# Kernel optimization log

Measured on AMD Instinct MI355X. Metric: run time of the kernel, lower is better.

Reference implementation:

```python
import jax, jax.numpy as jnp
import numpy as np

N = 20000      # nodes
E = 120000     # directed edges (self-loops added in reference, per PyG default)
F_IN = 235
HID = 256
HEADS = 8
NEG_SLOPE = 0.2


def setup_inputs() -> dict:
    key = jax.random.key(0)
    ks = jax.random.split(key, 24)
    p = lambda k, shape: (jax.random.normal(k, shape, jnp.float32) * 0.05)
    inp = {}
    inp["x"] = jax.random.normal(ks[0], (N, F_IN), jnp.float32)
    inp["edge_index"] = jax.random.randint(ks[1], (2, E), 0, N, jnp.int32)
    # input projection
    inp["w_in"] = p(ks[2], (F_IN, HID)); inp["b_in"] = jnp.zeros((HID,), jnp.float32)
    # temporal MLP
    inp["w_t1"] = p(ks[3], (HID, HID)); inp["b_t1"] = jnp.zeros((HID,), jnp.float32)
    inp["w_t2"] = p(ks[4], (HID, HID)); inp["b_t2"] = jnp.zeros((HID,), jnp.float32)
    # GAT layer 1: heads=8, out_per_head=32, concat -> 256
    C1 = HID // HEADS
    inp["w_g1"] = p(ks[5], (HID, HEADS * C1)); inp["a_src1"] = p(ks[6], (HEADS, C1))
    inp["a_dst1"] = p(ks[7], (HEADS, C1)); inp["b_g1"] = jnp.zeros((HEADS * C1,), jnp.float32)
    # GAT layer 2: same shape
    inp["w_g2"] = p(ks[8], (HID, HEADS * C1)); inp["a_src2"] = p(ks[9], (HEADS, C1))
    inp["a_dst2"] = p(ks[10], (HEADS, C1)); inp["b_g2"] = jnp.zeros((HEADS * C1,), jnp.float32)
    # GAT layer 3: heads=8, out_per_head=256, concat -> 2048
    inp["w_g3"] = p(ks[11], (HID, HEADS * HID)); inp["a_src3"] = p(ks[12], (HEADS, HID))
    inp["a_dst3"] = p(ks[13], (HEADS, HID)); inp["b_g3"] = jnp.zeros((HEADS * HID,), jnp.float32)
    # classifier
    inp["w_c1"] = p(ks[14], (2 * HID, HID)); inp["b_c1"] = jnp.zeros((HID,), jnp.float32)
    inp["w_c2"] = p(ks[15], (HID, 2)); inp["b_c2"] = jnp.zeros((2,), jnp.float32)
    return inp


def _gat(x, src, dst, W, a_src, a_dst, b, C):
    """PyG-style GATConv: gather -> per-edge logits -> segment softmax -> scatter-add."""
    h = (x @ W).reshape(-1, HEADS, C)                       # [N, H, C]
    alpha_s = jnp.sum(h * a_src, axis=-1)                   # [N, H]
    alpha_d = jnp.sum(h * a_dst, axis=-1)                   # [N, H]
    e = jax.nn.leaky_relu(alpha_s[src] + alpha_d[dst], NEG_SLOPE)   # [Etot, H]
    m = jax.ops.segment_max(e, dst, num_segments=N)         # [N, H] (self-loops ensure non-empty)
    ex = jnp.exp(e - m[dst])
    den = jax.ops.segment_sum(ex, dst, num_segments=N)
    alpha = ex / (den[dst] + 1e-16)                          # [Etot, H]
    out = jax.ops.segment_sum(alpha[:, :, None] * h[src], dst, num_segments=N)  # [N, H, C]
    return out.reshape(-1, HEADS * C) + b


def reference(x, edge_index, w_in, b_in, w_t1, b_t1, w_t2, b_t2,
              w_g1, a_src1, a_dst1, b_g1, w_g2, a_src2, a_dst2, b_g2,
              w_g3, a_src3, a_dst3, b_g3, w_c1, b_c1, w_c2, b_c2):
    h = jax.nn.elu(x @ w_in + b_in)                          # [N, 256]
    t = jax.nn.relu(h @ w_t1 + b_t1) @ w_t2 + b_t2          # [N, 256] (dropout inactive in eval)
    loop = jnp.arange(N, dtype=edge_index.dtype)
    src = jnp.concatenate([edge_index[0], loop])
    dst = jnp.concatenate([edge_index[1], loop])
    g = jax.nn.elu(_gat(h, src, dst, w_g1, a_src1, a_dst1, b_g1, HID // HEADS))
    g = jax.nn.elu(_gat(g, src, dst, w_g2, a_src2, a_dst2, b_g2, HID // HEADS))
    g = jax.nn.elu(_gat(g, src, dst, w_g3, a_src3, a_dst3, b_g3, HID))  # [N, 2048]
    g = g.reshape(N, HEADS, HID).mean(axis=1)                # [N, 256]
    comb = jnp.concatenate([g, t], axis=-1)                  # [N, 512]
    logits = jax.nn.relu(comb @ w_c1 + b_c1) @ w_c2 + b_c2   # [N, 2]
    return logits
```

## Files before the change

### kernel.cpp

```cpp
#include <hip/hip_runtime.h>
#include <hip/hip_bf16.h>
#include <math.h>


#define HID 256
#define HEADS 8
#define FIN 235

typedef __attribute__((ext_vector_type(8))) short short8;
typedef __attribute__((ext_vector_type(4))) float floatx4;

__device__ __forceinline__ float elu_f(float x) { return x > 0.f ? x : __expf(x) - 1.f; }
__device__ __forceinline__ float bf2f(unsigned short u) {
  return __uint_as_float(((unsigned int)u) << 16);
}
__device__ __forceinline__ unsigned short f2bfu(float f) {
  union { __hip_bfloat16 b; unsigned short u; } c;
  c.b = __float2bfloat16(f);
  return c.u;
}

__global__ void xcvt_k(const float* __restrict__ x, __hip_bfloat16* __restrict__ xb, int M) {
  int id = blockIdx.x * blockDim.x + threadIdx.x;
  if (id >= M * 256) return;
  int m = id >> 8, k = id & 255;
  xb[id] = (k < FIN) ? __float2bfloat16(x[(size_t)m * FIN + k]) : __float2bfloat16(0.f);
}

__global__ void wprep_k(const float* __restrict__ w_in, const float* __restrict__ w_t1,
                        const float* __restrict__ w_g1, const float* __restrict__ w_t2,
                        const float* __restrict__ w_g2, const float* __restrict__ w_c1,
                        const float* __restrict__ w_g3, const float* __restrict__ a_s3,
                        const float* __restrict__ a_d3, __hip_bfloat16* __restrict__ wtin,
                        __hip_bfloat16* __restrict__ wtpair, __hip_bfloat16* __restrict__ wtt2,
                        __hip_bfloat16* __restrict__ wtg2, __hip_bfloat16* __restrict__ wtc1,
                        __hip_bfloat16* __restrict__ wtg3s, float* __restrict__ apj) {
  __shared__ float t[32][33];
  int z = blockIdx.z;
  if (z == 14) {
    int idx = (blockIdx.y * 8 + blockIdx.x) * 256 + threadIdx.y * 32 + threadIdx.x;
    if (idx < 256 * 16) {
      int k = idx >> 4, o = idx & 15;
      int h = o >> 1;
      const float* av = (o & 1) ? (a_d3 + h * 256) : (a_s3 + h * 256);
      const float* wr = w_g3 + (size_t)k * 2048 + h * 256;
      float s = 0.f;
      for (int c = 0; c < 256; c++) s += wr[c] * av[c];
      apj[idx] = s;
    }
    return;
  }
  const float* src;
  __hip_bfloat16* dst;
  int K, Kpad, Nstride;
  if (z == 5) {
    src = w_c1; dst = wtc1; K = 512; Kpad = 512; Nstride = 256;
  } else {
    if (blockIdx.y >= 8) return;
    switch (z) {
      case 0: src = w_in; dst = wtin; K = FIN; Kpad = 256; Nstride = 256; break;
      case 1: src = w_t1; dst = wtpair; K = 256; Kpad = 256; Nstride = 256; break;
      case 2: src = w_g1; dst = wtpair + 256 * 256; K = 256; Kpad = 256; Nstride = 256; break;
      case 3: src = w_t2; dst = wtt2; K = 256; Kpad = 256; Nstride = 256; break;
      case 4: src = w_g2; dst = wtg2; K = 256; Kpad = 256; Nstride = 256; break;
      default: {
        int h = z - 6;
        src = w_g3 + h * 256; dst = wtg3s + h * 256; K = 256; Kpad = 2048; Nstride = 2048;
      }
    }
  }
  int nb = blockIdx.x * 32, kb = blockIdx.y * 32;
  int tx = threadIdx.x, ty = threadIdx.y;
#pragma unroll
  for (int j = 0; j < 32; j += 8) {
    int k = kb + ty + j;
    t[ty + j][tx] = (k < K) ? src[(size_t)k * Nstride + nb + tx] : 0.f;
  }
  __syncthreads();
#pragma unroll
  for (int j = 0; j < 32; j += 8) {
    int n = nb + ty + j;
    int k = kb + tx;
    dst[(size_t)n * Kpad + k] = __float2bfloat16(t[tx][ty + j]);
  }
}

__global__ void count_k(const int* __restrict__ ei, int* __restrict__ deg, int E) {
  int i = blockIdx.x * blockDim.x + threadIdx.x;
  if (i < E) atomicAdd(&deg[ei[E + i]], 1);
}

__global__ void scan_k(const int* __restrict__ deg, int* __restrict__ rp, int n) {
  __shared__ int wsum[16];
  __shared__ int s_carry;
  int tid = threadIdx.x, lane = tid & 63, wid = tid >> 6;
  if (tid == 0) { s_carry = 0; rp[0] = 0; }
  __syncthreads();
  for (int base = 0; base < n; base += 1024) {
    int i = base + tid;
    int x = (i < n) ? (deg[i] + 1) : 0;
#pragma unroll
    for (int off = 1; off < 64; off <<= 1) {
      int y = __shfl_up(x, off);
      if (lane >= off) x += y;
    }
    if (lane == 63) wsum[wid] = x;
    __syncthreads();
    if (wid == 0 && lane < 16) {
      int s = wsum[lane];
#pragma unroll
      for (int off = 1; off < 16; off <<= 1) {
        int y = __shfl_up(s, off);
        if (lane >= off) s += y;
      }
      wsum[lane] = s;
    }
    __syncthreads();
    int offset = s_carry + (wid > 0 ? wsum[wid - 1] : 0);
    if (i < n) rp[i + 1] = offset + x;
    __syncthreads();
    if (tid == 1023) s_carry += wsum[15];
    __syncthreads();
  }
}

__global__ void fill_k(const int* __restrict__ ei, const int* __restrict__ rp,
                       int* __restrict__ fillc, int* __restrict__ colA, int E, int n) {
  int i = blockIdx.x * blockDim.x + threadIdx.x;
  if (i < E) {
    int d = ei[E + i];
    int pos = rp[d] + atomicAdd(&fillc[d], 1);
    colA[pos] = ei[i];
  } else if (i < E + n) {
    int v = i - E;
    int pos = rp[v] + atomicAdd(&fillc[v], 1);
    colA[pos] = v;
  }
}

template <int ACT>
__global__ __launch_bounds__(256) void mgemm64_k(
    const __hip_bfloat16* __restrict__ A, const __hip_bfloat16* __restrict__ Bt,
    const float* __restrict__ bias, __hip_bfloat16* __restrict__ Cb,
    int ldc, int M, int N, int K) {
  __shared__ short As[64 * 40];
  __shared__ short Bs[64 * 40];
  int tid = threadIdx.x;
  int row0 = blockIdx.y * 64, col0 = blockIdx.x * 64;
  int w = tid >> 6, lane = tid & 63;
  int wr = w >> 1, wc = w & 1;
  int quad = lane >> 4, l16 = lane & 15;
  floatx4 zero = {0.f, 0.f, 0.f, 0.f};
  floatx4 acc[2][2];
#pragma unroll
  for (int i = 0; i < 2; i++)
#pragma unroll
    for (int j = 0; j < 2; j++) acc[i][j] = zero;

  int srow = tid >> 2, sq = tid & 3;
  const __hip_bfloat16* Ap = A + (size_t)(row0 + srow) * K + sq * 8;
  const __hip_bfloat16* Bp = Bt + (size_t)(col0 + srow) * K + sq * 8;
  bool aok = (row0 + srow) < M;

  uint4 a1 = make_uint4(0, 0, 0, 0);
  if (aok) a1 = *(const uint4*)(Ap);
  uint4 b1 = *(const uint4*)(Bp);

  for (int k0 = 0; k0 < K; k0 += 32) {
    __syncthreads();
    *(uint4*)&As[srow * 40 + sq * 8] = a1;
    *(uint4*)&Bs[srow * 40 + sq * 8] = b1;
    int kn = k0 + 32;
    if (kn < K) {
      if (aok) a1 = *(const uint4*)(Ap + kn);
      b1 = *(const uint4*)(Bp + kn);
    }
    __syncthreads();
    short8 fa[2], fb[2];
#pragma unroll
    for (int i = 0; i < 2; i++) {
      fa[i] = *(const short8*)&As[(wr * 32 + i * 16 + l16) * 40 + quad * 8];
      fb[i] = *(const short8*)&Bs[(wc * 32 + i * 16 + l16) * 40 + quad * 8];
    }
#pragma unroll
    for (int mi = 0; mi < 2; mi++)
#pragma unroll
      for (int ni = 0; ni < 2; ni++)
        acc[mi][ni] = __builtin_amdgcn_mfma_f32_16x16x32_bf16(fa[mi], fb[ni], acc[mi][ni], 0, 0, 0);
  }

#pragma unroll
  for (int mi = 0; mi < 2; mi++) {
    int rbase = row0 + wr * 32 + mi * 16 + quad * 4;
#pragma unroll
    for (int ni = 0; ni < 2; ni++) {
      int c = col0 + wc * 32 + ni * 16 + l16;
      float bv = bias ? bias[c] : 0.f;
#pragma unroll
      for (int reg = 0; reg < 4; reg++) {
        int rr = rbase + reg;
        if (rr >= M) continue;
        float v = acc[mi][ni][reg] + bv;
        if (ACT == 1) v = fmaxf(v, 0.f);
        if (ACT == 2) v = elu_f(v);
        Cb[(size_t)rr * ldc + c] = __float2bfloat16(v);
      }
    }
  }
}

__global__ __launch_bounds__(256) void mgemm_dual_k(
    const __hip_bfloat16* __restrict__ A, const __hip_bfloat16* __restrict__ Bt,
    const float* __restrict__ bias1, __hip_bfloat16* __restrict__ O1,
    __hip_bfloat16* __restrict__ O2, int M) {
  const int K = 256;
  __shared__ short As[64 * 40];
  __shared__ short Bs[128 * 40];
  int tid = threadIdx.x;
  int row0 = blockIdx.y * 64, col0 = blockIdx.x * 128;
  int w = tid >> 6, lane = tid & 63;
  int wr = w >> 1, wc = w & 1;
  int quad = lane >> 4, l16 = lane & 15;
  floatx4 zero = {0.f, 0.f, 0.f, 0.f};
  floatx4 acc[2][4];
#pragma unroll
  for (int i = 0; i < 2; i++)
#pragma unroll
    for (int j = 0; j < 4; j++) acc[i][j] = zero;

  int srow = tid >> 2, sq = tid & 3;
  const __hip_bfloat16* Ap = A + (size_t)(row0 + srow) * K + sq * 8;
  const __hip_bfloat16* Bp1 = Bt + (size_t)(col0 + srow) * K + sq * 8;
  const __hip_bfloat16* Bp2 = Bt + (size_t)(col0 + 64 + srow) * K + sq * 8;
  bool aok = (row0 + srow) < M;

  uint4 a1 = make_uint4(0, 0, 0, 0);
  if (aok) a1 = *(const uint4*)(Ap);
  uint4 b1 = *(const uint4*)(Bp1);
  uint4 b2 = *(const uint4*)(Bp2);

  for (int k0 = 0; k0 < K; k0 += 32) {
    __syncthreads();
    *(uint4*)&As[srow * 40 + sq * 8] = a1;
    *(uint4*)&Bs[srow * 40 + sq * 8] = b1;
    *(uint4*)&Bs[(64 + srow) * 40 + sq * 8] = b2;
    int kn = k0 + 32;
    if (kn < K) {
      if (aok) a1 = *(const uint4*)(Ap + kn);
      b1 = *(const uint4*)(Bp1 + kn);
      b2 = *(const uint4*)(Bp2 + kn);
    }
    __syncthreads();
    short8 fa[2], fb[4];
#pragma unroll
    for (int i = 0; i < 2; i++)
      fa[i] = *(const short8*)&As[(wr * 32 + i * 16 + l16) * 40 + quad * 8];
#pragma unroll
    for (int i = 0; i < 4; i++)
      fb[i] = *(const short8*)&Bs[(wc * 64 + i * 16 + l16) * 40 + quad * 8];
#pragma unroll
    for (int mi = 0; mi < 2; mi++)
#pragma unroll
      for (int ni = 0; ni < 4; ni++)
        acc[mi][ni] = __builtin_amdgcn_mfma_f32_16x16x32_bf16(fa[mi], fb[ni], acc[mi][ni], 0, 0, 0);
  }

#pragma unroll
  for (int mi = 0; mi < 2; mi++) {
    int rbase = row0 + wr * 32 + mi * 16 + quad * 4;
#pragma unroll
    for (int ni = 0; ni < 4; ni++) {
      int c = col0 + wc * 64 + ni * 16 + l16;
      bool first = c < 256;
      float bv = first ? bias1[c] : 0.f;
      int cc = first ? c : (c - 256);
#pragma unroll
      for (int reg = 0; reg < 4; reg++) {
        int rr = rbase + reg;
        if (rr >= M) continue;
        float v = acc[mi][ni][reg] + bv;
        if (first) v = fmaxf(v, 0.f);
        __hip_bfloat16* dst = first ? O1 : O2;
        dst[(size_t)rr * 256 + cc] = __float2bfloat16(v);
      }
    }
  }
}

__global__ __launch_bounds__(512) void mgemm3_k(
    const __hip_bfloat16* __restrict__ A, const __hip_bfloat16* __restrict__ Bt,
    const float* __restrict__ bias, __hip_bfloat16* __restrict__ comb, int M) {
  const int K = 2048;
  __shared__ short As[64 * 40];
  __shared__ short Bs[256 * 40];
  int tid = threadIdx.x;
  int row0 = blockIdx.x * 64;
  int w = tid >> 6, lane = tid & 63;
  int wr = w & 3, wc = w >> 2;
  int quad = lane >> 4, l16 = lane & 15;
  floatx4 acc[8], sum[8];
#pragma unroll
  for (int i = 0; i < 8; i++) {
    acc[i] = (floatx4){0.f, 0.f, 0.f, 0.f};
    sum[i] = (floatx4){0.f, 0.f, 0.f, 0.f};
  }

  bool at = tid < 256;
  int arow = tid >> 2, achk = (tid & 3) * 8;
  const __hip_bfloat16* Ap = A + (size_t)(row0 + arow) * K + achk;
  bool aok = at && (row0 + arow) < M;
  int brow = tid >> 1, boff = (tid & 1) * 16;
  const __hip_bfloat16* Bp = Bt + (size_t)brow * K + boff;

  uint4 a1 = make_uint4(0, 0, 0, 0);
  if (aok) a1 = *(const uint4*)(Ap);
  uint4 b1 = *(const uint4*)(Bp);
  uint4 b2 = *(const uint4*)(Bp + 8);

  for (int k0 = 0; k0 < K; k0 += 32) {
    __syncthreads();
    if (at) *(uint4*)&As[arow * 40 + achk] = a1;
    *(uint4*)&Bs[brow * 40 + boff] = b1;
    *(uint4*)&Bs[brow * 40 + boff + 8] = b2;
    int kn = k0 + 32;
    if (kn < K) {
      if (aok) a1 = *(const uint4*)(Ap + kn);
      b1 = *(const uint4*)(Bp + kn);
      b2 = *(const uint4*)(Bp + kn + 8);
    }
    __syncthreads();
    short8 fa = *(const short8*)&As[(wr * 16 + l16) * 40 + quad * 8];
#pragma unroll
    for (int ni = 0; ni < 8; ni++) {
      short8 fb = *(const short8*)&Bs[(wc * 128 + ni * 16 + l16) * 40 + quad * 8];
      acc[ni] = __builtin_amdgcn_mfma_f32_16x16x32_bf16(fa, fb, acc[ni], 0, 0, 0);
    }
    if (((k0 + 32) & 255) == 0) {
      int h = k0 >> 8;
#pragma unroll
      for (int ni = 0; ni < 8; ni++) {
        int c = wc * 128 + ni * 16 + l16;
        float bv = bias[h * 256 + c];
#pragma unroll
        for (int reg = 0; reg < 4; reg++) {
          sum[ni][reg] += elu_f(acc[ni][reg] + bv);
          acc[ni][reg] = 0.f;
        }
      }
    }
  }

  int rbase = row0 + wr * 16 + quad * 4;
#pragma unroll
  for (int ni = 0; ni < 8; ni++) {
    int c = wc * 128 + ni * 16 + l16;
#pragma unroll
    for (int reg = 0; reg < 4; reg++) {
      int rr = rbase + reg;
      if (rr >= M) continue;
      comb[(size_t)rr * 512 + c] = __float2bfloat16(sum[ni][reg] * 0.125f);
    }
  }
}

__global__ __launch_bounds__(512) void mgemm_cls_k(
    const __hip_bfloat16* __restrict__ A, const __hip_bfloat16* __restrict__ Bt,
    const float* __restrict__ bias, const float* __restrict__ w2,
    const float* __restrict__ b2f, float* __restrict__ out, int M) {
  const int K = 512;
  __shared__ short As[64 * 40];
  __shared__ short Bs[256 * 40];
  __shared__ float ls[64][2][2];
  int tid = threadIdx.x;
  int row0 = blockIdx.x * 64;
  int w = tid >> 6, lane = tid & 63;
  int wr = w & 3, wc = w >> 2;
  int quad = lane >> 4, l16 = lane & 15;
  floatx4 acc[8];
#pragma unroll
  for (int i = 0; i < 8; i++) acc[i] = (floatx4){0.f, 0.f, 0.f, 0.f};

  bool at = tid < 256;
  int arow = tid >> 2, achk = (tid & 3) * 8;
  const __hip_bfloat16* Ap = A + (size_t)(row0 + arow) * K + achk;
  bool aok = at && (row0 + arow) < M;
  int brow = tid >> 1, boff = (tid & 1) * 16;
  const __hip_bfloat16* Bp = Bt + (size_t)brow * K + boff;

  uint4 a1 = make_uint4(0, 0, 0, 0);
  if (aok) a1 = *(const uint4*)(Ap);
  uint4 b1 = *(const uint4*)(Bp);
  uint4 b2 = *(const uint4*)(Bp + 8);

  for (int k0 = 0; k0 < K; k0 += 32) {
    __syncthreads();
    if (at) *(uint4*)&As[arow * 40 + achk] = a1;
    *(uint4*)&Bs[brow * 40 + boff] = b1;
    *(uint4*)&Bs[brow * 40 + boff + 8] = b2;
    int kn = k0 + 32;
    if (kn < K) {
      if (aok) a1 = *(const uint4*)(Ap + kn);
      b1 = *(const uint4*)(Bp + kn);
      b2 = *(const uint4*)(Bp + kn + 8);
    }
    __syncthreads();
    short8 fa = *(const short8*)&As[(wr * 16 + l16) * 40 + quad * 8];
#pragma unroll
    for (int ni = 0; ni < 8; ni++) {
      short8 fb = *(const short8*)&Bs[(wc * 128 + ni * 16 + l16) * 40 + quad * 8];
      acc[ni] = __builtin_amdgcn_mfma_f32_16x16x32_bf16(fa, fb, acc[ni], 0, 0, 0);
    }
  }

  float p0[4] = {0.f, 0.f, 0.f, 0.f}, p1[4] = {0.f, 0.f, 0.f, 0.f};
#pragma unroll
  for (int ni = 0; ni < 8; ni++) {
    int c = wc * 128 + ni * 16 + l16;
    float bv = bias[c];
    float w20 = w2[c * 2 + 0], w21 = w2[c * 2 + 1];
#pragma unroll
    for (int reg = 0; reg < 4; reg++) {
      float v = fmaxf(acc[ni][reg] + bv, 0.f);
      p0[reg] += v * w20;
      p1[reg] += v * w21;
    }
  }
#pragma unroll
  for (int off = 1; off < 16; off <<= 1)
#pragma unroll
    for (int reg = 0; reg < 4; reg++) {
      p0[reg] += __shfl_xor(p0[reg], off);
      p1[reg] += __shfl_xor(p1[reg], off);
    }
  if (l16 == 0) {
#pragma unroll
    for (int reg = 0; reg < 4; reg++) {
      int rl = wr * 16 + quad * 4 + reg;
      ls[rl][wc][0] = p0[reg];
      ls[rl][wc][1] = p1[reg];
    }
  }
  __syncthreads();
  if (tid < 64) {
    int r = row0 + tid;
    if (r < M) {
      out[r * 2 + 0] = ls[tid][0][0] + ls[tid][1][0] + b2f[0];
      out[r * 2 + 1] = ls[tid][0][1] + ls[tid][1][1] + b2f[1];
    }
  }
}

__global__ __launch_bounds__(256) void alpha3_k(const __hip_bfloat16* __restrict__ g2,
                                                const float* __restrict__ apj,
                                                float* __restrict__ as_, float* __restrict__ ad_,
                                                int M) {
  __shared__ float sapj[4096];
  int tid = threadIdx.x;
  for (int i = tid; i < 4096; i += 256) sapj[i] = apj[i];
  __syncthreads();
  int nl = tid >> 4, o = tid & 15;
  int n = blockIdx.x * 16 + nl;
  if (n >= M) return;
  const __hip_bfloat16* row = g2 + (size_t)n * 256;
  float s = 0.f;
  for (int cc = 0; cc < 256; cc += 8) {
    short8 v8 = *(const short8*)(row + cc);
#pragma unroll
    for (int j = 0; j < 8; j++)
      s += bf2f((unsigned short)v8[j]) * sapj[(cc + j) * 16 + o];
  }
  if (o & 1) ad_[n * 8 + (o >> 1)] = s;
  else as_[n * 8 + (o >> 1)] = s;
}

__global__ void alpha_small_k(const __hip_bfloat16* __restrict__ hW, const float* __restrict__ a_s,
                              const float* __restrict__ a_d, float* __restrict__ as_,
                              float* __restrict__ ad_, int M) {
  int idx = blockIdx.x * blockDim.x + threadIdx.x;
  if (idx >= M * HEADS) return;
  int h = idx & 7;
  const __hip_bfloat16* row = hW + (size_t)(idx >> 3) * HID + h * 32;
  const float* ws = a_s + h * 32;
  const float* wd = a_d + h * 32;
  float s = 0.f, d = 0.f;
#pragma unroll
  for (int cc = 0; cc < 32; cc += 8) {
    short8 v8 = *(const short8*)(row + cc);
#pragma unroll
    for (int j = 0; j < 8; j++) {
      float v = bf2f((unsigned short)v8[j]);
      s += v * ws[cc + j];
      d += v * wd[cc + j];
    }
  }
  as_[idx] = s;
  ad_[idx] = d;
}

__global__ __launch_bounds__(256) void aggf_k(const int* __restrict__ rp,
                                              const int* __restrict__ col,
                                              const __hip_bfloat16* __restrict__ hW,
                                              const float* __restrict__ as_,
                                              const float* __restrict__ ad_,
                                              const float* __restrict__ bias,
                                              __hip_bfloat16* __restrict__ out, int M) {
  int dst = blockIdx.x * 4 + (threadIdx.x >> 6);
  if (dst >= M) return;
  int t = threadIdx.x & 63;
  int h = t >> 3, c = t << 2;
  int beg = rp[dst], end = rp[dst + 1];
  float adv = ad_[dst * 8 + h];
  float m = -3.4e38f;
  for (int i = beg; i < end; i++) {
    float e = as_[col[i] * 8 + h] + adv;
    e = e > 0.f ? e : 0.2f * e;
    m = fmaxf(m, e);
  }
  float den = 0.f;
  float a0 = 0.f, a1 = 0.f, a2 = 0.f, a3 = 0.f;
  for (int i = beg; i < end; i++) {
    int s = col[i];
    float e = as_[s * 8 + h] + adv;
    e = e > 0.f ? e : 0.2f * e;
    float ex = __expf(e - m);
    den += ex;
    union { uint2 u; unsigned short us[4]; } uu;
    uu.u = *(const uint2*)(hW + (size_t)s * HID + c);
    a0 += ex * bf2f(uu.us[0]);
    a1 += ex * bf2f(uu.us[1]);
    a2 += ex * bf2f(uu.us[2]);
    a3 += ex * bf2f(uu.us[3]);
  }
  float inv = 1.f / (den + 1e-16f);
  out[(size_t)dst * HID + c + 0] = __float2bfloat16(elu_f(a0 * inv + bias[c + 0]));
  out[(size_t)dst * HID + c + 1] = __float2bfloat16(elu_f(a1 * inv + bias[c + 1]));
  out[(size_t)dst * HID + c + 2] = __float2bfloat16(elu_f(a2 * inv + bias[c + 2]));
  out[(size_t)dst * HID + c + 3] = __float2bfloat16(elu_f(a3 * inv + bias[c + 3]));
}

__global__ __launch_bounds__(256) void esoft_k(const int* __restrict__ rp,
                                               const int* __restrict__ col,
                                               const float* __restrict__ as_,
                                               const float* __restrict__ ad_,
                                               float* __restrict__ ex,
                                               float* __restrict__ invden, int M) {
  int dst = blockIdx.x * 4 + (threadIdx.x >> 6);
  if (dst >= M) return;
  int lane = threadIdx.x & 63;
  int es = lane >> 3, h = lane & 7;
  int beg = rp[dst], end = rp[dst + 1];
  float adv = ad_[dst * 8 + h];
  float m = -3.4e38f;
  for (int i = beg + es; i < end; i += 8) {
    float e = as_[col[i] * 8 + h] + adv;
    e = e > 0.f ? e : 0.2f * e;
    m = fmaxf(m, e);
  }
  m = fmaxf(m, __shfl_xor(m, 8));
  m = fmaxf(m, __shfl_xor(m, 16));
  m = fmaxf(m, __shfl_xor(m, 32));
  float den = 0.f;
  for (int i = beg + es; i < end; i += 8) {
    float e = as_[col[i] * 8 + h] + adv;
    e = e > 0.f ? e : 0.2f * e;
    float v = __expf(e - m);
    ex[(size_t)i * 8 + h] = v;
    den += v;
  }
  den += __shfl_xor(den, 8);
  den += __shfl_xor(den, 16);
  den += __shfl_xor(den, 32);
  if (es == 0) invden[dst * 8 + h] = 1.f / (den + 1e-16f);
}

__global__ __launch_bounds__(256) void agg3_k(const int* __restrict__ rp,
                                              const int* __restrict__ col,
                                              const __hip_bfloat16* __restrict__ g2,
                                              const float* __restrict__ ex,
                                              const float* __restrict__ invden,
                                              __hip_bfloat16* __restrict__ outA, int M) {
  int dst = blockIdx.x * 4 + (threadIdx.x >> 6);
  if (dst >= M) return;
  int t = threadIdx.x & 63;
  int beg = rp[dst], end = rp[dst + 1];
  float acc[4][8];
#pragma unroll
  for (int ch = 0; ch < 4; ch++)
#pragma unroll
    for (int h = 0; h < 8; h++) acc[ch][h] = 0.f;
  for (int i = beg; i < end; i++) {
    int s = col[i];
    float4 w0 = *(const float4*)(ex + (size_t)i * 8);
    float4 w1 = *(const float4*)(ex + (size_t)i * 8 + 4);
    union { uint2 u; unsigned short us[4]; } uu;
    uu.u = *(const uint2*)(g2 + (size_t)s * 256 + t * 4);
#pragma unroll
    for (int ch = 0; ch < 4; ch++) {
      float v = bf2f(uu.us[ch]);
      acc[ch][0] += w0.x * v; acc[ch][1] += w0.y * v;
      acc[ch][2] += w0.z * v; acc[ch][3] += w0.w * v;
      acc[ch][4] += w1.x * v; acc[ch][5] += w1.y * v;
      acc[ch][6] += w1.z * v; acc[ch][7] += w1.w * v;
    }
  }
#pragma unroll
  for (int h = 0; h < 8; h++) {
    float inv = invden[dst * 8 + h];
    union { uint2 u; unsigned short us[4]; } pk;
#pragma unroll
    for (int ch = 0; ch < 4; ch++) pk.us[ch] = f2bfu(acc[ch][h] * inv);
    *(uint2*)(outA + (size_t)dst * 2048 + h * 256 + t * 4) = pk.u;
  }
}

extern "C" void kernel_launch(void* const* d_in, const int* in_sizes, int n_in,
                              void* d_out, int out_size, void* d_ws, size_t ws_size,
                              hipStream_t stream) {
  const float* x      = (const float*)d_in[0];
  const int*   ei     = (const int*)d_in[1];
  const float* w_in   = (const float*)d_in[2];
  const float* b_in   = (const float*)d_in[3];
  const float* w_t1   = (const float*)d_in[4];
  const float* b_t1   = (const float*)d_in[5];
  const float* w_t2   = (const float*)d_in[6];
  const float* b_t2   = (const float*)d_in[7];
  const float* w_g1   = (const float*)d_in[8];
  const float* a_src1 = (const float*)d_in[9];
  const float* a_dst1 = (const float*)d_in[10];
  const float* b_g1   = (const float*)d_in[11];
  const float* w_g2   = (const float*)d_in[12];
  const float* a_src2 = (const float*)d_in[13];
  const float* a_dst2 = (const float*)d_in[14];
  const float* b_g2   = (const float*)d_in[15];
  const float* w_g3   = (const float*)d_in[16];
  const float* a_src3 = (const float*)d_in[17];
  const float* a_dst3 = (const float*)d_in[18];
  const float* b_g3   = (const float*)d_in[19];
  const float* w_c1   = (const float*)d_in[20];
  const float* b_c1   = (const float*)d_in[21];
  const float* w_c2   = (const float*)d_in[22];
  const float* b_c2   = (const float*)d_in[23];
  const int M = in_sizes[0] / FIN;
  const int E = in_sizes[1] / 2;
  (void)n_in; (void)out_size; (void)ws_size;

  char* wsb = (char*)d_ws;
  size_t off = 0;
  auto alloc = [&](size_t bytes) {
    void* p = wsb + off;
    off = (off + bytes + 255) & ~(size_t)255;
    return p;
  };
  typedef __hip_bfloat16 bf;
  bf* xb     = (bf*)alloc((size_t)M * 256 * 2);
  bf* wtin   = (bf*)alloc(256 * 256 * 2);
  bf* wtpair = (bf*)alloc(512 * 256 * 2);
  bf* wtt2   = (bf*)alloc(256 * 256 * 2);
  bf* wtg2   = (bf*)alloc(256 * 256 * 2);
  bf* wtg3s  = (bf*)alloc(256 * 2048 * 2);
  bf* wtc1   = (bf*)alloc(256 * 512 * 2);
  bf* actA   = (bf*)alloc((size_t)M * HID * 2);
  bf* actB   = (bf*)alloc((size_t)M * HID * 2);
  bf* hW1    = (bf*)alloc((size_t)M * HID * 2);
  bf* comb   = (bf*)alloc((size_t)M * 2 * HID * 2);
  bf* hWb    = (bf*)alloc((size_t)M * 2048 * 2);
  float* as_ = (float*)alloc((size_t)M * 8 * 4);
  float* ad_ = (float*)alloc((size_t)M * 8 * 4);
  float* apj = (float*)alloc(256 * 16 * 4);
  float* exw = (float*)alloc((size_t)(E + M) * 8 * 4);
  float* ivd = (float*)alloc((size_t)M * 8 * 4);
  int* degfill = (int*)alloc((size_t)2 * M * 4);
  int* deg   = degfill;
  int* fillc = degfill + M;
  int* rp    = (int*)alloc((size_t)(M + 1) * 4);
  int* colA  = (int*)alloc((size_t)(E + M) * 4);

  xcvt_k<<<(M * 256 + 255) / 256, 256, 0, stream>>>(x, xb, M);
  wprep_k<<<dim3(8, 16, 15), dim3(32, 8), 0, stream>>>(
      w_in, w_t1, w_g1, w_t2, w_g2, w_c1, w_g3, a_src3, a_dst3,
      wtin, wtpair, wtt2, wtg2, wtc1, wtg3s, apj);

  hipMemsetAsync(degfill, 0, (size_t)2 * M * 4, stream);
  count_k<<<(E + 255) / 256, 256, 0, stream>>>(ei, deg, E);
  scan_k<<<1, 1024, 0, stream>>>(deg, rp, M);
  fill_k<<<(E + M + 255) / 256, 256, 0, stream>>>(ei, rp, fillc, colA, E, M);

  int eg = (M + 3) / 4;
  int mg = (M + 63) / 64;

  mgemm64_k<2><<<dim3(4, mg), 256, 0, stream>>>(xb, wtin, b_in, actA, HID, M, HID, 256);
  mgemm_dual_k<<<dim3(4, mg), 256, 0, stream>>>(actA, wtpair, b_t1, actB, hW1, M);
  mgemm64_k<0><<<dim3(4, mg), 256, 0, stream>>>(actB, wtt2, b_t2, comb + HID, 2 * HID, M, HID, 256);

  alpha_small_k<<<(M * 8 + 255) / 256, 256, 0, stream>>>(hW1, a_src1, a_dst1, as_, ad_, M);
  aggf_k<<<eg, 256, 0, stream>>>(rp, colA, hW1, as_, ad_, b_g1, actB, M);

  mgemm64_k<0><<<dim3(4, mg), 256, 0, stream>>>(actB, wtg2, nullptr, hW1, HID, M, HID, 256);
  alpha_small_k<<<(M * 8 + 255) / 256, 256, 0, stream>>>(hW1, a_src2, a_dst2, as_, ad_, M);
  aggf_k<<<eg, 256, 0, stream>>>(rp, colA, hW1, as_, ad_, b_g2, actA, M);

  alpha3_k<<<(M + 15) / 16, 256, 0, stream>>>(actA, apj, as_, ad_, M);
  esoft_k<<<eg, 256, 0, stream>>>(rp, colA, as_, ad_, exw, ivd, M);
  agg3_k<<<eg, 256, 0, stream>>>(rp, colA, actA, exw, ivd, hWb, M);
  mgemm3_k<<<mg, 512, 0, stream>>>(hWb, wtg3s, b_g3, comb, M);

  mgemm_cls_k<<<mg, 512, 0, stream>>>(comb, wtc1, b_c1, w_c2, b_c2, (float*)d_out, M);
}
```

Measured before the change: 435.7 us.

## Fuse GAT attention-score projections into GEMM epilogues and retile layer-3 GEMM

Computes per-head source/destination attention scores for GAT layers 1 and 2 directly from the GEMM accumulators using wave shuffles, removing the separate alpha kernels and their reread of the projected features. The layer-3 GEMM is retiled from 64x256 tiles with 512 threads to 64x64 tiles with 256 threads over a 2D grid, giving more blocks for the GPU at the cost of re-reading the A operand four times. Scores now come from fp32 accumulators rather than bf16-rounded values.

```diff
diff --git a/kernel.cpp b/kernel.cpp
--- a/kernel.cpp
+++ b/kernel.cpp
@@ -138,11 +138,12 @@
   }
 }
 
-template <int ACT>
+template <int ACT, int ALPHA>
 __global__ __launch_bounds__(256) void mgemm64_k(
     const __hip_bfloat16* __restrict__ A, const __hip_bfloat16* __restrict__ Bt,
     const float* __restrict__ bias, __hip_bfloat16* __restrict__ Cb,
-    int ldc, int M, int N, int K) {
+    int ldc, int M, int N, int K, const float* __restrict__ a_s,
+    const float* __restrict__ a_d, float* __restrict__ as_, float* __restrict__ ad_) {
   __shared__ short As[64 * 40];
   __shared__ short Bs[64 * 40];
   int tid = threadIdx.x;
@@ -207,12 +208,38 @@
       }
     }
   }
+
+  if (ALPHA) {
+    int h = 2 * blockIdx.x + wc;
+    float aS0 = a_s[h * 32 + l16], aS1 = a_s[h * 32 + 16 + l16];
+    float aD0 = a_d[h * 32 + l16], aD1 = a_d[h * 32 + 16 + l16];
+#pragma unroll
+    for (int mi = 0; mi < 2; mi++)
+#pragma unroll
+      for (int reg = 0; reg < 4; reg++) {
+        float pS = acc[mi][0][reg] * aS0 + acc[mi][1][reg] * aS1;
+        float pD = acc[mi][0][reg] * aD0 + acc[mi][1][reg] * aD1;
+#pragma unroll
+        for (int off = 1; off < 16; off <<= 1) {
+          pS += __shfl_xor(pS, off);
+          pD += __shfl_xor(pD, off);
+        }
+        if (l16 == 0) {
+          int r = row0 + wr * 32 + mi * 16 + quad * 4 + reg;
+          if (r < M) {
+            as_[r * 8 + h] = pS;
+            ad_[r * 8 + h] = pD;
+          }
+        }
+      }
+  }
 }
 
 __global__ __launch_bounds__(256) void mgemm_dual_k(
     const __hip_bfloat16* __restrict__ A, const __hip_bfloat16* __restrict__ Bt,
     const float* __restrict__ bias1, __hip_bfloat16* __restrict__ O1,
-    __hip_bfloat16* __restrict__ O2, int M) {
+    __hip_bfloat16* __restrict__ O2, int M, const float* __restrict__ a_s1,
+    const float* __restrict__ a_d1, float* __restrict__ as_, float* __restrict__ ad_) {
   const int K = 256;
   __shared__ short As[64 * 40];
   __shared__ short Bs[128 * 40];
@@ -285,80 +312,118 @@
       }
     }
   }
-}
-
-__global__ __launch_bounds__(512) void mgemm3_k(
+
+  if (blockIdx.x >= 2) {
+    int hb = (blockIdx.x - 2) * 4 + wc * 2;
+    float aSA0 = a_s1[hb * 32 + l16], aSA1 = a_s1[hb * 32 + 16 + l16];
+    float aDA0 = a_d1[hb * 32 + l16], aDA1 = a_d1[hb * 32 + 16 + l16];
+    float aSB0 = a_s1[(hb + 1) * 32 + l16], aSB1 = a_s1[(hb + 1) * 32 + 16 + l16];
+    float aDB0 = a_d1[(hb + 1) * 32 + l16], aDB1 = a_d1[(hb + 1) * 32 + 16 + l16];
+#pragma unroll
+    for (int mi = 0; mi < 2; mi++)
+#pragma unroll
+      for (int reg = 0; reg < 4; reg++) {
+        float pSA = acc[mi][0][reg] * aSA0 + acc[mi][1][reg] * aSA1;
+        float pDA = acc[mi][0][reg] * aDA0 + acc[mi][1][reg] * aDA1;
+        float pSB = acc[mi][2][reg] * aSB0 + acc[mi][3][reg] * aSB1;
+        float pDB = acc[mi][2][reg] * aDB0 + acc[mi][3][reg] * aDB1;
+#pragma unroll
+        for (int off = 1; off < 16; off <<= 1) {
+          pSA += __shfl_xor(pSA, off);
+          pDA += __shfl_xor(pDA, off);
+          pSB += __shfl_xor(pSB, off);
+          pDB += __shfl_xor(pDB, off);
+        }
+        if (l16 == 0) {
+          int r = row0 + wr * 32 + mi * 16 + quad * 4 + reg;
+          if (r < M) {
+            as_[r * 8 + hb] = pSA;
+            ad_[r * 8 + hb] = pDA;
+            as_[r * 8 + hb + 1] = pSB;
+            ad_[r * 8 + hb + 1] = pDB;
+          }
+        }
+      }
+  }
+}
+
+__global__ __launch_bounds__(256) void mgemm3_k(
     const __hip_bfloat16* __restrict__ A, const __hip_bfloat16* __restrict__ Bt,
     const float* __restrict__ bias, __hip_bfloat16* __restrict__ comb, int M) {
   const int K = 2048;
   __shared__ short As[64 * 40];
-  __shared__ short Bs[256 * 40];
+  __shared__ short Bs[64 * 40];
   int tid = threadIdx.x;
-  int row0 = blockIdx.x * 64;
+  int row0 = blockIdx.y * 64, col0 = blockIdx.x * 64;
   int w = tid >> 6, lane = tid & 63;
-  int wr = w & 3, wc = w >> 2;
+  int wr = w >> 1, wc = w & 1;
   int quad = lane >> 4, l16 = lane & 15;
-  floatx4 acc[8], sum[8];
-#pragma unroll
-  for (int i = 0; i < 8; i++) {
-    acc[i] = (floatx4){0.f, 0.f, 0.f, 0.f};
-    sum[i] = (floatx4){0.f, 0.f, 0.f, 0.f};
-  }
-
-  bool at = tid < 256;
-  int arow = tid >> 2, achk = (tid & 3) * 8;
-  const __hip_bfloat16* Ap = A + (size_t)(row0 + arow) * K + achk;
-  bool aok = at && (row0 + arow) < M;
-  int brow = tid >> 1, boff = (tid & 1) * 16;
-  const __hip_bfloat16* Bp = Bt + (size_t)brow * K + boff;
+  floatx4 zero = {0.f, 0.f, 0.f, 0.f};
+  floatx4 acc[2][2], sum[2][2];
+#pragma unroll
+  for (int i = 0; i < 2; i++)
+#pragma unroll
+    for (int j = 0; j < 2; j++) { acc[i][j] = zero; sum[i][j] = zero; }
+
+  int srow = tid >> 2, sq = tid & 3;
+  const __hip_bfloat16* Ap = A + (size_t)(row0 + srow) * K + sq * 8;
+  const __hip_bfloat16* Bp = Bt + (size_t)(col0 + srow) * K + sq * 8;
+  bool aok = (row0 + srow) < M;
 
   uint4 a1 = make_uint4(0, 0, 0, 0);
   if (aok) a1 = *(const uint4*)(Ap);
   uint4 b1 = *(const uint4*)(Bp);
-  uint4 b2 = *(const uint4*)(Bp + 8);
 
   for (int k0 = 0; k0 < K; k0 += 32) {
     __syncthreads();
-    if (at) *(uint4*)&As[arow * 40 + achk] = a1;
-    *(uint4*)&Bs[brow * 40 + boff] = b1;
-    *(uint4*)&Bs[brow * 40 + boff + 8] = b2;
+    *(uint4*)&As[srow * 40 + sq * 8] = a1;
+    *(uint4*)&Bs[srow * 40 + sq * 8] = b1;
     int kn = k0 + 32;
     if (kn < K) {
       if (aok) a1 = *(const uint4*)(Ap + kn);
       b1 = *(const uint4*)(Bp + kn);
-      b2 = *(const uint4*)(Bp + kn + 8);
-    }
-    __syncthreads();
-    short8 fa = *(const short8*)&As[(wr * 16 + l16) * 40 + quad * 8];
-#pragma unroll
-    for (int ni = 0; ni < 8; ni++) {
-      short8 fb = *(const short8*)&Bs[(wc * 128 + ni * 16 + l16) * 40 + quad * 8];
-      acc[ni] = __builtin_amdgcn_mfma_f32_16x16x32_bf16(fa, fb, acc[ni], 0, 0, 0);
-    }
+    }
+    __syncthreads();
+    short8 fa[2], fb[2];
+#pragma unroll
+    for (int i = 0; i < 2; i++) {
+      fa[i] = *(const short8*)&As[(wr * 32 + i * 16 + l16) * 40 + quad * 8];
+      fb[i] = *(const short8*)&Bs[(wc * 32 + i * 16 + l16) * 40 + quad * 8];
+    }
+#pragma unroll
+    for (int mi = 0; mi < 2; mi++)
+#pragma unroll
+      for (int ni = 0; ni < 2; ni++)
+        acc[mi][ni] = __builtin_amdgcn_mfma_f32_16x16x32_bf16(fa[mi], fb[ni], acc[mi][ni], 0, 0, 0);
     if (((k0 + 32) & 255) == 0) {
       int h = k0 >> 8;
 #pragma unroll
-      for (int ni = 0; ni < 8; ni++) {
-        int c = wc * 128 + ni * 16 + l16;
-        float bv = bias[h * 256 + c];
-#pragma unroll
-        for (int reg = 0; reg < 4; reg++) {
-          sum[ni][reg] += elu_f(acc[ni][reg] + bv);
-          acc[ni][reg] = 0.f;
+      for (int mi = 0; mi < 2; mi++)
+#pragma unroll
+        for (int ni = 0; ni < 2; ni++) {
+          int c = col0 + wc * 32 + ni * 16 + l16;
+          float bv = bias[h * 256 + c];
+#pragma unroll
+          for (int reg = 0; reg < 4; reg++) {
+            sum[mi][ni][reg] += elu_f(acc[mi][ni][reg] + bv);
+            acc[mi][ni][reg] = 0.f;
+          }
         }
+    }
+  }
+
+#pragma unroll
+  for (int mi = 0; mi < 2; mi++) {
+    int rbase = row0 + wr * 32 + mi * 16 + quad * 4;
+#pragma unroll
+    for (int ni = 0; ni < 2; ni++) {
+      int c = col0 + wc * 32 + ni * 16 + l16;
+#pragma unroll
+      for (int reg = 0; reg < 4; reg++) {
+        int rr = rbase + reg;
+        if (rr >= M) continue;
+        comb[(size_t)rr * 512 + c] = __float2bfloat16(sum[mi][ni][reg] * 0.125f);
       }
-    }
-  }
-
-  int rbase = row0 + wr * 16 + quad * 4;
-#pragma unroll
-  for (int ni = 0; ni < 8; ni++) {
-    int c = wc * 128 + ni * 16 + l16;
-#pragma unroll
-    for (int reg = 0; reg < 4; reg++) {
-      int rr = rbase + reg;
-      if (rr >= M) continue;
-      comb[(size_t)rr * 512 + c] = __float2bfloat16(sum[ni][reg] * 0.125f);
     }
   }
 }
@@ -471,30 +536,6 @@
   }
   if (o & 1) ad_[n * 8 + (o >> 1)] = s;
   else as_[n * 8 + (o >> 1)] = s;
-}
-
-__global__ void alpha_small_k(const __hip_bfloat16* __restrict__ hW, const float* __restrict__ a_s,
-                              const float* __restrict__ a_d, float* __restrict__ as_,
-                              float* __restrict__ ad_, int M) {
-  int idx = blockIdx.x * blockDim.x + threadIdx.x;
-  if (idx >= M * HEADS) return;
-  int h = idx & 7;
-  const __hip_bfloat16* row = hW + (size_t)(idx >> 3) * HID + h * 32;
-  const float* ws = a_s + h * 32;
-  const float* wd = a_d + h * 32;
-  float s = 0.f, d = 0.f;
-#pragma unroll
-  for (int cc = 0; cc < 32; cc += 8) {
-    short8 v8 = *(const short8*)(row + cc);
-#pragma unroll
-    for (int j = 0; j < 8; j++) {
-      float v = bf2f((unsigned short)v8[j]);
-      s += v * ws[cc + j];
-      d += v * wd[cc + j];
-    }
-  }
-  as_[idx] = s;
-  ad_[idx] = d;
 }
 
 __global__ __launch_bounds__(256) void aggf_k(const int* __restrict__ rp,
@@ -688,21 +729,23 @@
   int eg = (M + 3) / 4;
   int mg = (M + 63) / 64;
 
-  mgemm64_k<2><<<dim3(4, mg), 256, 0, stream>>>(xb, wtin, b_in, actA, HID, M, HID, 256);
-  mgemm_dual_k<<<dim3(4, mg), 256, 0, stream>>>(actA, wtpair, b_t1, actB, hW1, M);
-  mgemm64_k<0><<<dim3(4, mg), 256, 0, stream>>>(actB, wtt2, b_t2, comb + HID, 2 * HID, M, HID, 256);
-
-  alpha_small_k<<<(M * 8 + 255) / 256, 256, 0, stream>>>(hW1, a_src1, a_dst1, as_, ad_, M);
+  mgemm64_k<2, 0><<<dim3(4, mg), 256, 0, stream>>>(xb, wtin, b_in, actA, HID, M, HID, 256,
+                                                   nullptr, nullptr, nullptr, nullptr);
+  mgemm_dual_k<<<dim3(4, mg), 256, 0, stream>>>(actA, wtpair, b_t1, actB, hW1, M,
+                                                a_src1, a_dst1, as_, ad_);
+  mgemm64_k<0, 0><<<dim3(4, mg), 256, 0, stream>>>(actB, wtt2, b_t2, comb + HID, 2 * HID,
+                                                   M, HID, 256, nullptr, nullptr, nullptr, nullptr);
+
   aggf_k<<<eg, 256, 0, stream>>>(rp, colA, hW1, as_, ad_, b_g1, actB, M);
 
-  mgemm64_k<0><<<dim3(4, mg), 256, 0, stream>>>(actB, wtg2, nullptr, hW1, HID, M, HID, 256);
-  alpha_small_k<<<(M * 8 + 255) / 256, 256, 0, stream>>>(hW1, a_src2, a_dst2, as_, ad_, M);
+  mgemm64_k<0, 1><<<dim3(4, mg), 256, 0, stream>>>(actB, wtg2, nullptr, hW1, HID, M, HID, 256,
+                                                   a_src2, a_dst2, as_, ad_);
   aggf_k<<<eg, 256, 0, stream>>>(rp, colA, hW1, as_, ad_, b_g2, actA, M);
 
   alpha3_k<<<(M + 15) / 16, 256, 0, stream>>>(actA, apj, as_, ad_, M);
   esoft_k<<<eg, 256, 0, stream>>>(rp, colA, as_, ad_, exw, ivd, M);
   agg3_k<<<eg, 256, 0, stream>>>(rp, colA, actA, exw, ivd, hWb, M);
-  mgemm3_k<<<mg, 512, 0, stream>>>(hWb, wtg3s, b_g3, comb, M);
+  mgemm3_k<<<dim3(4, mg), 256, 0, stream>>>(hWb, wtg3s, b_g3, comb, M);
 
   mgemm_cls_k<<<mg, 512, 0, stream>>>(comb, wtc1, b_c1, w_c2, b_c2, (float*)d_out, M);
 }
```

Result: faster. 417.7 us (-4.1%).
